# Kernel tuning notes

Hardware: AMD Instinct MI355X
Metric: run time of the kernel (lower is better)

Reference implementation:

```python
import math
import jax, jax.numpy as jnp
import numpy as np

B, T, N, S, D, H = 16, 64, 64, 4, 128, 8  # batch, enc steps, agents, state dim, lstm dim, heads


def _lin(k, i, o):
    return (jax.random.normal(k, (i, o), jnp.float32) / np.sqrt(i)).astype(jnp.float32)


def setup_inputs() -> dict:
    key = jax.random.key(0)
    ks = jax.random.split(key, 24)
    inp = {
        "x": jax.random.normal(ks[0], (B, T + 1, N, S), jnp.float32),
        # state_enc: S -> D
        "W_se": _lin(ks[1], S, D), "b_se": jnp.zeros((D,), jnp.float32),
        # init_hidden: S -> D (lstm_num = 1)
        "W_init": _lin(ks[2], S, D), "b_init": jnp.zeros((D,), jnp.float32),
        # GRU (1 layer): input D, hidden D; gates packed [r|z|n]
        "W_ih": _lin(ks[3], D, 3 * D), "W_hh": _lin(ks[4], D, 3 * D),
        "b_ih": jnp.zeros((3 * D,), jnp.float32), "b_hh": jnp.zeros((3 * D,), jnp.float32),
        # key_ct/query_ct/value_ct: D -> D, no bias (final_bias=False)
        "W_kc": _lin(ks[5], D, D), "W_qc": _lin(ks[6], D, D), "W_vc": _lin(ks[7], D, D),
        # gat attention: 2D -> 1
        "W_att": _lin(ks[8], 2 * D, 1), "b_att": jnp.zeros((1,), jnp.float32),
        # value: D -> D
        "W_val": _lin(ks[9], D, D), "b_val": jnp.zeros((D,), jnp.float32),
        # dec: 2D -> D
        "W_dec": _lin(ks[10], 2 * D, D), "b_dec": jnp.zeros((D,), jnp.float32),
        # mu/sig heads: D -> S
        "W_mu": _lin(ks[11], D, S), "b_mu": jnp.zeros((S,), jnp.float32),
        "W_sig": _lin(ks[12], D, S), "b_sig": jnp.zeros((S,), jnp.float32),
    }
    return inp


def _gru(xs, h0, W_ih, W_hh, b_ih, b_hh):
    # xs: [T, BN, D]; h0: [BN, D]. PyTorch GRU gate math.
    def step(h, x_t):
        gi = x_t @ W_ih + b_ih
        gh = h @ W_hh + b_hh
        ir, iz, inn = jnp.split(gi, 3, axis=-1)
        hr, hz, hn = jnp.split(gh, 3, axis=-1)
        r = jax.nn.sigmoid(ir + hr)
        z = jax.nn.sigmoid(iz + hz)
        n = jnp.tanh(inn + r * hn)
        h_new = (1.0 - z) * n + z * h
        return h_new, h_new
    hT, ys = jax.lax.scan(step, h0, xs)
    return ys, hT


def reference(x, W_se, b_se, W_init, b_init, W_ih, W_hh, b_ih, b_hh,
              W_kc, W_qc, W_vc, W_att, b_att, W_val, b_val,
              W_dec, b_dec, W_mu, b_mu, W_sig, b_sig):
    Bn, T1, Nn, Sn = x.shape
    Tn = T1 - 1
    Dn = W_se.shape[1]
    hd = Dn // H
    BN = Bn * Nn

    # initialize: h0 from first frame
    h0 = x[:, 0].reshape(BN, Sn) @ W_init + b_init  # [BN, D]

    # encode: state_enc + GRU over time
    xe = x[:, :-1] @ W_se + b_se                     # [B, T, N, D]
    xs = jnp.transpose(xe, (1, 0, 2, 3)).reshape(Tn, BN, Dn)
    ys, hT = _gru(xs, h0, W_ih, W_hh, b_ih, b_hh)    # ys: [T, BN, D]
    out = ys.reshape(Tn, Bn, Nn, Dn)

    # extract: per-pair temporal attention (pa=True)
    k = (out @ W_kc).reshape(Tn, Bn, Nn, H, hd)
    q = (out @ W_qc).reshape(Tn, Bn, Nn, H, hd)
    v = (out @ W_vc).reshape(Tn, Bn, Nn, H, hd)
    # score[b,h,i,j,t] = q[t,b,j]·k[t,b,i] / sqrt(D); softmax over t
    score = jnp.einsum('tbjhd,tbihd->bhijt', q, k) / math.sqrt(Dn)
    a = jax.nn.softmax(score, axis=-1)
    ctx = jnp.einsum('bhijt,tbihd->bhijd', a, v)     # [B,H,N,N,hd]
    ctx = jnp.transpose(ctx, (0, 2, 3, 1, 4)).reshape(Bn, Nn, Nn, Dn)

    # gat edge weight with tanh activation and zeroed diagonal
    w = jnp.concatenate([ctx, jnp.swapaxes(ctx, 1, 2)], axis=-1)  # [B,N,N,2D]
    e = (w @ W_att + b_att)[..., 0]
    weight = jnp.tanh(e + 0.5) * (1.0 - jnp.eye(Nn, dtype=x.dtype))

    # decode one step with last frame
    xd = (x[:, -1].reshape(BN, Sn) @ W_se + b_se)[None]  # [1, BN, D]
    _, h2 = _gru(xd, hT, W_ih, W_hh, b_ih, b_hh)
    bvec = h2.reshape(Bn, Nn, Dn)
    vv = bvec @ W_val + b_val
    p = jnp.einsum('bij,bjd->bid', weight, vv) / Nn      # gat: divide by agent_num
    c = jnp.concatenate([vv, p], axis=-1)
    d = c @ W_dec + b_dec
    mu = d @ W_mu + b_mu
    sig = jax.nn.sigmoid(d @ W_sig + b_sig) + 1e-6       # reg_norm = 1.0
    return mu, sig
```

## Files before the change

### kernel.cpp

```cpp
#include <hip/hip_runtime.h>
#include <math.h>

#define Bb 16
#define Tt 64
#define Nn 64
#define Ss 4
#define Dd 128
#define Hh 8
#define HD 16
#define BN 1024
#define G3 384

#define OFF_WX   0
#define OFF_BX   1536
#define OFF_YS   4096
#define OFF_KH   (OFF_YS + Tt*BN*Dd)
#define OFF_QH   (OFF_KH + Bb*Hh*Tt*Nn*HD/2)
#define OFF_VW1  (OFF_QH + Bb*Hh*Tt*Nn*HD/2)
#define OFF_VW2  (OFF_VW1 + Bb*Hh*Tt*Nn)
#define OFF_E    (OFF_VW2 + Bb*Hh*Tt*Nn)
#define OFF_VV   (OFF_E + Bb*Nn*Nn)
#define OFF_WKQ  (OFF_VV + BN*Dd)
#define OFF_WT   (OFF_WKQ + 17408)
#define OFF_WDF  (OFF_WT + 24576)
#define OFF_WMF  (OFF_WDF + 16384)
#define WS_FLOATS (OFF_WMF + 1024)

typedef _Float16 half2_t __attribute__((ext_vector_type(2)));
typedef _Float16 f16x8 __attribute__((ext_vector_type(8)));
typedef float f32x4 __attribute__((ext_vector_type(4)));

__device__ __forceinline__ float fast_sigmoid(float v) {
  return 1.f / (1.f + __expf(-v));
}
__device__ __forceinline__ float fast_tanh(float v) {
  float e2 = __expf(2.f * v);
  return 1.f - 2.f / (e2 + 1.f);
}

__global__ __launch_bounds__(384) void k_precompute(
    const float* __restrict__ W_se, const float* __restrict__ b_se,
    const float* __restrict__ W_ih, const float* __restrict__ b_ih,
    const float* __restrict__ W_hh,
    const float* __restrict__ W_kc, const float* __restrict__ W_qc,
    const float* __restrict__ W_vc, const float* __restrict__ W_att,
    const float* __restrict__ W_dec, const float* __restrict__ W_mu,
    const float* __restrict__ W_sig,
    float* __restrict__ ws) {
  const int tid = threadIdx.x;
  if (blockIdx.x == 50) {
    _Float16* WF = (_Float16*)(ws + OFF_WMF);
    for (int idx = tid; idx < 4*64*8; idx += 384) {
      int ks = idx >> 9, l = (idx >> 3) & 63, j = idx & 7;
      int k = ks*32 + (l >> 4)*8 + j;
      int c16 = l & 15;
      float v = (c16 < 4) ? W_mu[(size_t)k*Ss + c16]
              : ((c16 < 8) ? W_sig[(size_t)k*Ss + c16 - 4] : 0.f);
      WF[(size_t)(ks*64 + l)*8 + j] = (_Float16)v;
    }
    return;
  }
  if (blockIdx.x >= 42) {
    const int nt = blockIdx.x - 42;
    _Float16* WF = (_Float16*)(ws + OFF_WDF);
    for (int idx = tid; idx < 8*64*8; idx += 384) {
      int ks = idx >> 9, l = (idx >> 3) & 63, j = idx & 7;
      int k = ks*32 + (l >> 4)*8 + j;
      int c = nt*16 + (l & 15);
      WF[(size_t)((nt*8 + ks)*64 + l)*8 + j] = (_Float16)W_dec[(size_t)k*Dd + c];
    }
    return;
  }
  if (blockIdx.x >= 25) {
    const int nt = blockIdx.x - 25;
    _Float16* WF = (_Float16*)(ws + OFF_WKQ);
    for (int idx = tid; idx < 4*64*8; idx += 384) {
      int ks = idx >> 9, l = (idx >> 3) & 63, j = idx & 7;
      int k = ks*32 + (l >> 4)*8 + j;
      int c16 = l & 15;
      float v;
      if (nt < 16) {
        int cg = nt*16 + c16;
        v = (cg < Dd) ? W_kc[(size_t)k*Dd + cg] : W_qc[(size_t)k*Dd + cg - Dd];
      } else {
        int h = c16 >> 1, which = c16 & 1;
        float s = 0.f;
        for (int d = 0; d < HD; ++d)
          s = fmaf(W_vc[(size_t)k*Dd + h*HD + d], W_att[which*Dd + h*HD + d], s);
        v = s;
      }
      WF[(size_t)((nt*4 + ks)*64 + l)*8 + j] = (_Float16)v;
    }
    return;
  }
  if (blockIdx.x > 0) {
    const int nt = blockIdx.x - 1;
    _Float16* WF = (_Float16*)(ws + OFF_WT);
    for (int idx = tid; idx < 4*64*8; idx += 384) {
      int ks = idx >> 9, l = (idx >> 3) & 63, j = idx & 7;
      int k = ks*32 + (l >> 4)*8 + j;
      int c = nt*16 + (l & 15);
      WF[(size_t)((nt*4 + ks)*64 + l)*8 + j] = (_Float16)W_hh[(size_t)k*G3 + c];
    }
    return;
  }
  const int c = tid;
  float* Wx = ws + OFF_WX; float* bx = ws + OFF_BX;
  float accb = b_ih[c];
  float a0 = 0.f, a1 = 0.f, a2 = 0.f, a3 = 0.f;
  for (int k = 0; k < Dd; ++k) {
    float w = W_ih[k*G3 + c];
    accb = fmaf(b_se[k], w, accb);
    a0 = fmaf(W_se[0*Dd + k], w, a0);
    a1 = fmaf(W_se[1*Dd + k], w, a1);
    a2 = fmaf(W_se[2*Dd + k], w, a2);
    a3 = fmaf(W_se[3*Dd + k], w, a3);
  }
  bx[c] = accb;
  Wx[0*G3 + c] = a0; Wx[1*G3 + c] = a1; Wx[2*G3 + c] = a2; Wx[3*G3 + c] = a3;
}

__global__ __launch_bounds__(512, 2) void k_gru(
    const float* __restrict__ x, const float* __restrict__ W_init,
    const float* __restrict__ b_init,
    const float* __restrict__ b_hh, float* __restrict__ ws) {
  __shared__ __align__(16) _Float16 h_l[4][Dd + 8];
  __shared__ float gg[4][G3];
  __shared__ float xt_l[Tt+1][4][Ss];
  const int tid = threadIdx.x;
  const int wave = tid >> 6;
  const int lane = tid & 63;
  const int l15 = lane & 15;
  const int lk = lane >> 4;
  const int blk = blockIdx.x;
  const int row0 = blk * 4;
  const int b = row0 >> 6;
  const int n0 = row0 & 63;
  float* ys = ws + OFF_YS;
  const float* Wx = ws + OFF_WX;
  const float* bxp = ws + OFF_BX;

  const f16x8* WF = (const f16x8*)(ws + OFF_WT);
  f16x8 wf[3][4];
  #pragma unroll
  for (int i = 0; i < 3; ++i)
    #pragma unroll
    for (int ks = 0; ks < 4; ++ks)
      wf[i][ks] = WF[(size_t)((wave*3 + i)*4 + ks)*64 + lane];
  float br[3];
  #pragma unroll
  for (int i = 0; i < 3; ++i) br[i] = b_hh[(wave*3 + i)*16 + l15];

  const int row = tid >> 7, d = tid & 127;
  float wxr[3][4], bx3[3];
  #pragma unroll
  for (int g = 0; g < 3; ++g) {
    bx3[g] = bxp[g*Dd + d];
    #pragma unroll
    for (int s = 0; s < 4; ++s) wxr[g][s] = Wx[s*G3 + g*Dd + d];
  }

  for (int idx = tid; idx < (Tt+1)*4*Ss; idx += 512) {
    int t = idx >> 4, r = (idx >> 2) & 3, s = idx & 3;
    xt_l[t][r][s] = x[((size_t)(b*(Tt+1) + t)*Nn + (n0 + r))*Ss + s];
  }
  __syncthreads();

  float hprev;
  {
    float h0 = b_init[d];
    #pragma unroll
    for (int s = 0; s < Ss; ++s)
      h0 = fmaf(xt_l[0][row][s], W_init[s*Dd + d], h0);
    hprev = h0;
    h_l[row][d] = (_Float16)h0;
  }
  __syncthreads();

  for (int t = 0; t < Tt; ++t) {
    f16x8 af[4];
    #pragma unroll
    for (int ks = 0; ks < 4; ++ks)
      af[ks] = *(const f16x8*)&h_l[l15 & 3][ks*32 + lk*8];
    #pragma unroll
    for (int i = 0; i < 3; ++i) {
      f32x4 acc = {br[i], br[i], br[i], br[i]};
      #pragma unroll
      for (int ks = 0; ks < 4; ++ks)
        acc = __builtin_amdgcn_mfma_f32_16x16x32_f16(af[ks], wf[i][ks], acc, 0, 0, 0);
      if (lane < 16) {
        const int col = (wave*3 + i)*16 + l15;
        gg[0][col] = acc[0];
        gg[1][col] = acc[1];
        gg[2][col] = acc[2];
        gg[3][col] = acc[3];
      }
    }
    __syncthreads();
    {
      float gi_r = bx3[0], gi_z = bx3[1], gi_n = bx3[2];
      #pragma unroll
      for (int s = 0; s < 4; ++s) {
        float xv = xt_l[t][row][s];
        gi_r = fmaf(xv, wxr[0][s], gi_r);
        gi_z = fmaf(xv, wxr[1][s], gi_z);
        gi_n = fmaf(xv, wxr[2][s], gi_n);
      }
      float rg = fast_sigmoid(gi_r + gg[row][d]);
      float zg = fast_sigmoid(gi_z + gg[row][Dd + d]);
      float ng = fast_tanh(fmaf(rg, gg[row][2*Dd + d], gi_n));
      float hnew = fmaf(zg, hprev - ng, ng);
      hprev = hnew;
      h_l[row][d] = (_Float16)hnew;
      ys[(size_t)(t*BN + row0 + row)*Dd + d] = hnew;
    }
    __syncthreads();
  }
}

__global__ __launch_bounds__(256, 2) void k_kqv(float* __restrict__ ws) {
  __shared__ __align__(16) _Float16 ysl[64][136];
  const int tid = threadIdx.x;
  const int blk = blockIdx.x;
  const int b = blk >> 6, t = blk & 63;
  const int wave = tid >> 6, lane = tid & 63;
  const int l15 = lane & 15, lk = lane >> 4;

  const f16x8* WKQ = (const f16x8*)(ws + OFF_WKQ);
  f16x8 bf0[4], bf1[4], bf2[4], bf3[4], bu[4];
  #pragma unroll
  for (int ks = 0; ks < 4; ++ks) {
    bf0[ks] = WKQ[(size_t)((wave*4 + 0)*4 + ks)*64 + lane];
    bf1[ks] = WKQ[(size_t)((wave*4 + 1)*4 + ks)*64 + lane];
    bf2[ks] = WKQ[(size_t)((wave*4 + 2)*4 + ks)*64 + lane];
    bf3[ks] = WKQ[(size_t)((wave*4 + 3)*4 + ks)*64 + lane];
    bu[ks]  = WKQ[(size_t)(16*4 + ks)*64 + lane];
  }

  const float* ysrc = ws + OFF_YS + ((size_t)t*BN + b*64)*Dd;
  for (int idx = tid; idx < 64*16; idx += 256) {
    int r = idx >> 4, k8 = (idx & 15) * 8;
    float4 v0 = *(const float4*)&ysrc[r*Dd + k8];
    float4 v1 = *(const float4*)&ysrc[r*Dd + k8 + 4];
    f16x8 hv;
    hv[0] = (_Float16)v0.x; hv[1] = (_Float16)v0.y;
    hv[2] = (_Float16)v0.z; hv[3] = (_Float16)v0.w;
    hv[4] = (_Float16)v1.x; hv[5] = (_Float16)v1.y;
    hv[6] = (_Float16)v1.z; hv[7] = (_Float16)v1.w;
    *(f16x8*)&ysl[r][k8] = hv;
  }
  __syncthreads();

  _Float16* khd = (_Float16*)(ws + OFF_KH);
  _Float16* qhd = (_Float16*)(ws + OFF_QH);

  #pragma unroll
  for (int mt = 0; mt < 4; ++mt) {
    f16x8 af[4];
    #pragma unroll
    for (int ks = 0; ks < 4; ++ks)
      af[ks] = *(const f16x8*)&ysl[mt*16 + l15][ks*32 + lk*8];
    f32x4 a0 = {0.f,0.f,0.f,0.f}, a1 = a0, a2 = a0, a3 = a0;
    #pragma unroll
    for (int ks = 0; ks < 4; ++ks) {
      a0 = __builtin_amdgcn_mfma_f32_16x16x32_f16(af[ks], bf0[ks], a0, 0, 0, 0);
      a1 = __builtin_amdgcn_mfma_f32_16x16x32_f16(af[ks], bf1[ks], a1, 0, 0, 0);
      a2 = __builtin_amdgcn_mfma_f32_16x16x32_f16(af[ks], bf2[ks], a2, 0, 0, 0);
      a3 = __builtin_amdgcn_mfma_f32_16x16x32_f16(af[ks], bf3[ks], a3, 0, 0, 0);
    }
    const int rowb = mt*16 + lk*4;
    #pragma unroll
    for (int nti = 0; nti < 4; ++nti) {
      f32x4 av = (nti == 0) ? a0 : (nti == 1) ? a1 : (nti == 2) ? a2 : a3;
      const int gc = wave*64 + nti*16 + l15;
      const int hh = (gc >> 4) & 7;
      const int dd2 = gc & 15;
      _Float16* base = (gc < Dd) ? khd : qhd;
      const size_t rowbase = ((size_t)(b*Hh + hh)*Tt + t)*Nn*HD;
      #pragma unroll
      for (int rg2 = 0; rg2 < 4; ++rg2)
        base[rowbase + (size_t)(rowb + rg2)*HD + dd2] = (_Float16)av[rg2];
    }
    if (wave == 3) {
      f32x4 au = {0.f,0.f,0.f,0.f};
      #pragma unroll
      for (int ks = 0; ks < 4; ++ks)
        au = __builtin_amdgcn_mfma_f32_16x16x32_f16(af[ks], bu[ks], au, 0, 0, 0);
      const int h = l15 >> 1, which = l15 & 1;
      float* vw = ws + (which ? OFF_VW2 : OFF_VW1) + ((size_t)(b*Hh + h)*Tt + t)*Nn;
      #pragma unroll
      for (int rg2 = 0; rg2 < 4; ++rg2)
        vw[rowb + rg2] = au[rg2];
    }
  }
}

__global__ __launch_bounds__(1024) void k_attn(float* __restrict__ ws) {
  __shared__ float vw1_l[Tt][Nn];
  __shared__ float vw2_l[Tt][Nn];
  const int tid = threadIdx.x;
  const int bh = blockIdx.x;
  const int b = bh >> 3;
  const int wave = tid >> 6;
  const int it = wave >> 2, jt = wave & 3;
  const int i0 = it*16, j0 = jt*16;
  const int lane = tid & 63;
  const int l15 = lane & 15, lk = lane >> 4;
  const _Float16* kh = (const _Float16*)(ws + OFF_KH) + (size_t)bh*Tt*Nn*HD;
  const _Float16* qh = (const _Float16*)(ws + OFF_QH) + (size_t)bh*Tt*Nn*HD;
  const float* vw1 = ws + OFF_VW1 + (size_t)bh*Tt*Nn;
  const float* vw2 = ws + OFF_VW2 + (size_t)bh*Tt*Nn;
  float* e = ws + OFF_E + (size_t)b*Nn*Nn;
  const float scale = 0.08838834764831845f;

  #pragma unroll
  for (int s = 0; s < 4; ++s) {
    int idx = tid + s*1024;
    ((float*)vw1_l)[idx] = vw1[idx];
    ((float*)vw2_l)[idx] = vw2[idx];
  }
  __syncthreads();

  float S[4] = {0.f,0.f,0.f,0.f};
  float A1[4] = {0.f,0.f,0.f,0.f};
  float A2[4] = {0.f,0.f,0.f,0.f};
  const bool realk = (lk < 2);

  #pragma unroll 4
  for (int t = 0; t < Tt; ++t) {
    f16x8 af = {0,0,0,0,0,0,0,0}, bf = {0,0,0,0,0,0,0,0};
    if (realk) {
      af = *(const f16x8*)&kh[((size_t)t*Nn + i0 + l15)*HD + lk*8];
      bf = *(const f16x8*)&qh[((size_t)t*Nn + j0 + l15)*HD + lk*8];
    }
    f32x4 sc = {0.f,0.f,0.f,0.f};
    sc = __builtin_amdgcn_mfma_f32_16x16x32_f16(af, bf, sc, 0, 0, 0);
    float4 w1 = *(const float4*)&vw1_l[t][i0 + lk*4];
    float4 w2 = *(const float4*)&vw2_l[t][i0 + lk*4];
    const float* w1p = (const float*)&w1;
    const float* w2p = (const float*)&w2;
    #pragma unroll
    for (int r = 0; r < 4; ++r) {
      float s = fminf(fmaxf(sc[r] * scale, -60.f), 60.f);
      float ee = __expf(s);
      S[r] += ee;
      A1[r] = fmaf(ee, w1p[r], A1[r]);
      A2[r] = fmaf(ee, w2p[r], A2[r]);
    }
  }
  {
    const int j = j0 + l15;
    #pragma unroll
    for (int r = 0; r < 4; ++r) {
      const int i = i0 + lk*4 + r;
      float inv = 1.f / S[r];
      atomicAdd(&e[i*Nn + j], A1[r] * inv);
      atomicAdd(&e[j*Nn + i], A2[r] * inv);
    }
  }
}

__global__ __launch_bounds__(384) void k_decode(
    const float* __restrict__ x, const float* __restrict__ W_hh,
    const float* __restrict__ b_hh, const float* __restrict__ W_val,
    const float* __restrict__ b_val, float* __restrict__ ws) {
  __shared__ float h_lds[4][Dd];
  __shared__ float g_lds[4][4*Dd];
  __shared__ float xt[4][Ss];
  const int tid = threadIdx.x;
  const int blk = blockIdx.x;
  const int row0 = blk * 4;
  const int b = row0 >> 6;
  const int n0 = row0 & 63;
  const float* ys = ws + OFF_YS;
  const float* Wx = ws + OFF_WX;
  const float* bxp = ws + OFF_BX;
  if (tid < Dd) {
    for (int r = 0; r < 4; ++r)
      h_lds[r][tid] = ys[(size_t)((Tt-1)*BN + row0 + r)*Dd + tid];
  }
  if (tid >= 320 && tid < 336) {
    int q = tid - 320; int r = q >> 2, s = q & 3;
    xt[r][s] = x[((size_t)(b*(Tt+1) + Tt)*Nn + (n0 + r))*Ss + s];
  }
  const int c = tid;
  const float bhh = b_hh[c];
  const float wx0 = Wx[0*G3 + c], wx1 = Wx[1*G3 + c], wx2 = Wx[2*G3 + c], wx3 = Wx[3*G3 + c];
  const float bxv = bxp[c];
  __syncthreads();
  float acc[4] = {bhh, bhh, bhh, bhh};
  for (int k = 0; k < Dd; k += 4) {
    float w0 = W_hh[(k+0)*G3 + c];
    float w1 = W_hh[(k+1)*G3 + c];
    float w2 = W_hh[(k+2)*G3 + c];
    float w3 = W_hh[(k+3)*G3 + c];
    #pragma unroll
    for (int r = 0; r < 4; ++r) {
      float4 hv = *(const float4*)&h_lds[r][k];
      acc[r] = fmaf(hv.x, w0, acc[r]);
      acc[r] = fmaf(hv.y, w1, acc[r]);
      acc[r] = fmaf(hv.z, w2, acc[r]);
      acc[r] = fmaf(hv.w, w3, acc[r]);
    }
  }
  float gi[4];
  #pragma unroll
  for (int r = 0; r < 4; ++r) {
    float g = bxv;
    g = fmaf(xt[r][0], wx0, g);
    g = fmaf(xt[r][1], wx1, g);
    g = fmaf(xt[r][2], wx2, g);
    g = fmaf(xt[r][3], wx3, g);
    gi[r] = g;
  }
  if (c < 2*Dd) {
    #pragma unroll
    for (int r = 0; r < 4; ++r) g_lds[r][c] = acc[r] + gi[r];
  } else {
    #pragma unroll
    for (int r = 0; r < 4; ++r) { g_lds[r][c] = gi[r]; g_lds[r][c + Dd] = acc[r]; }
  }
  __syncthreads();
  if (tid < Dd) {
    const int d = tid;
    #pragma unroll
    for (int r = 0; r < 4; ++r) {
      float rg = fast_sigmoid(g_lds[r][d]);
      float zg = fast_sigmoid(g_lds[r][Dd + d]);
      float ng = fast_tanh(fmaf(rg, g_lds[r][3*Dd + d], g_lds[r][2*Dd + d]));
      float hn = fmaf(zg, h_lds[r][d] - ng, ng);
      h_lds[r][d] = hn;
    }
  }
  __syncthreads();
  if (tid < Dd) {
    const int c2 = tid;
    for (int r = 0; r < 4; ++r) {
      float a = b_val[c2];
      for (int k = 0; k < Dd; k += 4) {
        float4 hv = *(const float4*)&h_lds[r][k];
        a = fmaf(hv.x, W_val[(k+0)*Dd + c2], a);
        a = fmaf(hv.y, W_val[(k+1)*Dd + c2], a);
        a = fmaf(hv.z, W_val[(k+2)*Dd + c2], a);
        a = fmaf(hv.w, W_val[(k+3)*Dd + c2], a);
      }
      ws[OFF_VV + (size_t)(row0 + r)*Dd + c2] = a;
    }
  }
}

__global__ __launch_bounds__(256) void k_final(
    const float* __restrict__ b_dec, const float* __restrict__ b_mu,
    const float* __restrict__ b_sig, const float* __restrict__ b_att,
    float* __restrict__ ws, float* __restrict__ out) {
  __shared__ __align__(16) _Float16 vvT[Dd][72];
  __shared__ __align__(16) _Float16 wl[16][72];
  __shared__ __align__(16) _Float16 A2[16][264];
  __shared__ __align__(16) _Float16 A3[16][136];
  const int tid = threadIdx.x;
  const int wave = tid >> 6, lane = tid & 63;
  const int l15 = lane & 15, lk = lane >> 4;
  const int blk = blockIdx.x;
  const int b = blk >> 2, iq = blk & 3, i0 = iq*16;
  const float* vv = ws + OFF_VV + (size_t)b*64*Dd;
  const float* e  = ws + OFF_E + (size_t)b*Nn*Nn;
  const float batt = b_att[0];

  for (int idx = tid; idx < 64*Dd/4; idx += 256) {
    int r = idx >> 5, k4 = (idx & 31)*4;
    float4 v = *(const float4*)&vv[r*Dd + k4];
    vvT[k4+0][r] = (_Float16)v.x;
    vvT[k4+1][r] = (_Float16)v.y;
    vvT[k4+2][r] = (_Float16)v.z;
    vvT[k4+3][r] = (_Float16)v.w;
    int rl = r - i0;
    if (rl >= 0 && rl < 16) {
      A2[rl][k4+0] = (_Float16)v.x;
      A2[rl][k4+1] = (_Float16)v.y;
      A2[rl][k4+2] = (_Float16)v.z;
      A2[rl][k4+3] = (_Float16)v.w;
    }
  }
  for (int idx = tid; idx < 16*64; idx += 256) {
    int il = idx >> 6, jj = idx & 63;
    int i = i0 + il;
    float v = (i == jj) ? 0.f : fast_tanh(e[i*Nn + jj] + batt + 0.5f);
    wl[il][jj] = (_Float16)v;
  }
  __syncthreads();

  {
    f16x8 a0 = *(const f16x8*)&wl[l15][lk*8];
    f16x8 a1 = *(const f16x8*)&wl[l15][32 + lk*8];
    #pragma unroll
    for (int q = 0; q < 2; ++q) {
      const int nt = wave*2 + q;
      f16x8 b0 = *(const f16x8*)&vvT[nt*16 + l15][lk*8];
      f16x8 b1 = *(const f16x8*)&vvT[nt*16 + l15][32 + lk*8];
      f32x4 acc = {0.f,0.f,0.f,0.f};
      acc = __builtin_amdgcn_mfma_f32_16x16x32_f16(a0, b0, acc, 0, 0, 0);
      acc = __builtin_amdgcn_mfma_f32_16x16x32_f16(a1, b1, acc, 0, 0, 0);
      #pragma unroll
      for (int r = 0; r < 4; ++r)
        A2[lk*4 + r][128 + nt*16 + l15] = (_Float16)(acc[r] * (1.f/64.f));
    }
  }
  __syncthreads();

  const f16x8* WDF = (const f16x8*)(ws + OFF_WDF);
  {
    f16x8 ad[8];
    #pragma unroll
    for (int ks = 0; ks < 8; ++ks)
      ad[ks] = *(const f16x8*)&A2[l15][ks*32 + lk*8];
    #pragma unroll
    for (int q = 0; q < 2; ++q) {
      const int nt = wave*2 + q;
      const float bias = b_dec[nt*16 + l15];
      f32x4 acc = {bias, bias, bias, bias};
      #pragma unroll
      for (int ks = 0; ks < 8; ++ks)
        acc = __builtin_amdgcn_mfma_f32_16x16x32_f16(
            ad[ks], WDF[(size_t)((nt*8 + ks)*64) + lane], acc, 0, 0, 0);
      #pragma unroll
      for (int r = 0; r < 4; ++r)
        A3[lk*4 + r][nt*16 + l15] = (_Float16)acc[r];
    }
  }
  __syncthreads();

  if (wave == 0) {
    const f16x8* WMF = (const f16x8*)(ws + OFF_WMF);
    f16x8 ah[4];
    #pragma unroll
    for (int ks = 0; ks < 4; ++ks)
      ah[ks] = *(const f16x8*)&A3[l15][ks*32 + lk*8];
    const float bias = (l15 < 4) ? b_mu[l15] : ((l15 < 8) ? b_sig[l15 - 4] : 0.f);
    f32x4 acc = {bias, bias, bias, bias};
    #pragma unroll
    for (int ks = 0; ks < 4; ++ks)
      acc = __builtin_amdgcn_mfma_f32_16x16x32_f16(
          ah[ks], WMF[(size_t)(ks*64) + lane], acc, 0, 0, 0);
    if (l15 < 8) {
      const int which = l15 >> 2, s = l15 & 3;
      #pragma unroll
      for (int r = 0; r < 4; ++r) {
        float v = acc[r];
        if (which) v = 1.f/(1.f + __expf(-v)) + 1e-6f;
        out[(size_t)which*(Bb*Nn*Ss) + (size_t)(b*64 + i0 + lk*4 + r)*Ss + s] = v;
      }
    }
  }
}

extern "C" void kernel_launch(void* const* d_in, const int* in_sizes, int n_in,
                              void* d_out, int out_size, void* d_ws, size_t ws_size,
                              hipStream_t stream) {
  const float* x     = (const float*)d_in[0];
  const float* W_se  = (const float*)d_in[1];
  const float* b_se  = (const float*)d_in[2];
  const float* W_init= (const float*)d_in[3];
  const float* b_init= (const float*)d_in[4];
  const float* W_ih  = (const float*)d_in[5];
  const float* W_hh  = (const float*)d_in[6];
  const float* b_ih  = (const float*)d_in[7];
  const float* b_hh  = (const float*)d_in[8];
  const float* W_kc  = (const float*)d_in[9];
  const float* W_qc  = (const float*)d_in[10];
  const float* W_vc  = (const float*)d_in[11];
  const float* W_att = (const float*)d_in[12];
  const float* b_att = (const float*)d_in[13];
  const float* W_val = (const float*)d_in[14];
  const float* b_val = (const float*)d_in[15];
  const float* W_dec = (const float*)d_in[16];
  const float* b_dec = (const float*)d_in[17];
  const float* W_mu  = (const float*)d_in[18];
  const float* b_mu  = (const float*)d_in[19];
  const float* W_sig = (const float*)d_in[20];
  const float* b_sig = (const float*)d_in[21];
  float* ws = (float*)d_ws;
  float* out = (float*)d_out;

  if (ws_size < (size_t)WS_FLOATS * sizeof(float)) return;

  hipMemsetAsync(ws + OFF_E, 0, (size_t)Bb*Nn*Nn*sizeof(float), stream);
  k_precompute<<<51, 384, 0, stream>>>(W_se, b_se, W_ih, b_ih, W_hh, W_kc, W_qc,
                                       W_vc, W_att, W_dec, W_mu, W_sig, ws);
  k_gru<<<BN/4, 512, 0, stream>>>(x, W_init, b_init, b_hh, ws);
  k_kqv<<<Bb*Tt, 256, 0, stream>>>(ws);
  k_attn<<<Bb*Hh, 1024, 0, stream>>>(ws);
  k_decode<<<BN/4, 384, 0, stream>>>(x, W_hh, b_hh, W_val, b_val, ws);
  k_final<<<Bb*4, 256, 0, stream>>>(b_dec, b_mu, b_sig, b_att, ws, out);
}
```

Baseline: 139.1 us.

## Restructure GRU to 2 rows per block with in-register gate math and fp16 ys

The GRU recurrence kernel now handles 2 rows per 256-thread block instead of 4 rows per 512 threads, giving 512 blocks. Each wave computes two column tiles for all three gates, and the gate nonlinearities are applied straight from MFMA accumulators. This removes the gg LDS round trip and one __syncthreads per step, and double-buffers the hidden state. The ys history is now stored as fp16, which halves its write and read traffic, and k_kqv and k_decode read it directly without conversion. In exchange, only a quarter of the lanes do the elementwise work, the MFMA rows are mostly padding, and ys carries less precision.

Result: slower. 175.1 us (+25.9%).

```diff
diff --git a/kernel.cpp b/kernel.cpp
--- a/kernel.cpp
+++ b/kernel.cpp
@@ -120,99 +120,113 @@
   Wx[0*G3 + c] = a0; Wx[1*G3 + c] = a1; Wx[2*G3 + c] = a2; Wx[3*G3 + c] = a3;
 }
 
-__global__ __launch_bounds__(512, 2) void k_gru(
+__global__ __launch_bounds__(256, 2) void k_gru(
     const float* __restrict__ x, const float* __restrict__ W_init,
     const float* __restrict__ b_init,
     const float* __restrict__ b_hh, float* __restrict__ ws) {
-  __shared__ __align__(16) _Float16 h_l[4][Dd + 8];
-  __shared__ float gg[4][G3];
-  __shared__ float xt_l[Tt+1][4][Ss];
+  __shared__ __align__(16) _Float16 h_l[2][2][160];
+  __shared__ float xt_l[Tt+1][2][Ss];
   const int tid = threadIdx.x;
   const int wave = tid >> 6;
   const int lane = tid & 63;
-  const int l15 = lane & 15;
-  const int lk = lane >> 4;
+  const int l15 = lane & 15, lk = lane >> 4;
   const int blk = blockIdx.x;
-  const int row0 = blk * 4;
-  const int b = row0 >> 6;
-  const int n0 = row0 & 63;
-  float* ys = ws + OFF_YS;
+  const int row0 = blk * 2;
+  const int b = row0 >> 6, n0 = row0 & 63;
+  _Float16* ys = (_Float16*)(ws + OFF_YS);
   const float* Wx = ws + OFF_WX;
   const float* bxp = ws + OFF_BX;
 
   const f16x8* WF = (const f16x8*)(ws + OFF_WT);
-  f16x8 wf[3][4];
+  f16x8 wf[3][2][4];
+  float br[3][2], bx3[3][2], wxr[3][2][4];
   #pragma unroll
-  for (int i = 0; i < 3; ++i)
+  for (int g = 0; g < 3; ++g)
+    #pragma unroll
+    for (int u = 0; u < 2; ++u) {
+      const int nt = g*8 + wave*2 + u;
+      #pragma unroll
+      for (int ks = 0; ks < 4; ++ks)
+        wf[g][u][ks] = WF[(size_t)((nt*4 + ks)*64) + lane];
+      const int c = g*Dd + (wave*2 + u)*16 + l15;
+      br[g][u] = b_hh[c];
+      bx3[g][u] = bxp[c];
+      #pragma unroll
+      for (int s = 0; s < 4; ++s) wxr[g][u][s] = Wx[s*G3 + c];
+    }
+
+  for (int idx = tid; idx < (Tt+1)*2*Ss; idx += 256) {
+    int t = idx >> 3, r = (idx >> 2) & 1, s = idx & 3;
+    xt_l[t][r][s] = x[((size_t)(b*(Tt+1) + t)*Nn + (n0 + r))*Ss + s];
+  }
+  __syncthreads();
+
+  float hprev[2][2] = {{0.f,0.f},{0.f,0.f}};
+  if (lk == 0) {
+    #pragma unroll
+    for (int u = 0; u < 2; ++u) {
+      const int d = wave*32 + u*16 + l15;
+      #pragma unroll
+      for (int r = 0; r < 2; ++r) {
+        float h0 = b_init[d];
+        #pragma unroll
+        for (int s = 0; s < Ss; ++s)
+          h0 = fmaf(xt_l[0][r][s], W_init[s*Dd + d], h0);
+        hprev[u][r] = h0;
+        h_l[0][r][d] = (_Float16)h0;
+      }
+    }
+  }
+  __syncthreads();
+
+  for (int t = 0; t < Tt; ++t) {
+    const int cur = t & 1, nxt = cur ^ 1;
+    f16x8 af[4];
     #pragma unroll
     for (int ks = 0; ks < 4; ++ks)
-      wf[i][ks] = WF[(size_t)((wave*3 + i)*4 + ks)*64 + lane];
-  float br[3];
-  #pragma unroll
-  for (int i = 0; i < 3; ++i) br[i] = b_hh[(wave*3 + i)*16 + l15];
-
-  const int row = tid >> 7, d = tid & 127;
-  float wxr[3][4], bx3[3];
-  #pragma unroll
-  for (int g = 0; g < 3; ++g) {
-    bx3[g] = bxp[g*Dd + d];
-    #pragma unroll
-    for (int s = 0; s < 4; ++s) wxr[g][s] = Wx[s*G3 + g*Dd + d];
-  }
-
-  for (int idx = tid; idx < (Tt+1)*4*Ss; idx += 512) {
-    int t = idx >> 4, r = (idx >> 2) & 3, s = idx & 3;
-    xt_l[t][r][s] = x[((size_t)(b*(Tt+1) + t)*Nn + (n0 + r))*Ss + s];
-  }
-  __syncthreads();
-
-  float hprev;
-  {
-    float h0 = b_init[d];
-    #pragma unroll
-    for (int s = 0; s < Ss; ++s)
-      h0 = fmaf(xt_l[0][row][s], W_init[s*Dd + d], h0);
-    hprev = h0;
-    h_l[row][d] = (_Float16)h0;
-  }
-  __syncthreads();
-
-  for (int t = 0; t < Tt; ++t) {
-    f16x8 af[4];
-    #pragma unroll
-    for (int ks = 0; ks < 4; ++ks)
-      af[ks] = *(const f16x8*)&h_l[l15 & 3][ks*32 + lk*8];
-    #pragma unroll
-    for (int i = 0; i < 3; ++i) {
-      f32x4 acc = {br[i], br[i], br[i], br[i]};
-      #pragma unroll
-      for (int ks = 0; ks < 4; ++ks)
-        acc = __builtin_amdgcn_mfma_f32_16x16x32_f16(af[ks], wf[i][ks], acc, 0, 0, 0);
-      if (lane < 16) {
-        const int col = (wave*3 + i)*16 + l15;
-        gg[0][col] = acc[0];
-        gg[1][col] = acc[1];
-        gg[2][col] = acc[2];
-        gg[3][col] = acc[3];
+      af[ks] = *(const f16x8*)&h_l[cur][l15 & 1][ks*32 + lk*8];
+    f32x4 a00 = {br[0][0],br[0][0],br[0][0],br[0][0]};
+    f32x4 a01 = {br[0][1],br[0][1],br[0][1],br[0][1]};
+    f32x4 a10 = {br[1][0],br[1][0],br[1][0],br[1][0]};
+    f32x4 a11 = {br[1][1],br[1][1],br[1][1],br[1][1]};
+    f32x4 a20 = {br[2][0],br[2][0],br[2][0],br[2][0]};
+    f32x4 a21 = {br[2][1],br[2][1],br[2][1],br[2][1]};
+    #pragma unroll
+    for (int ks = 0; ks < 4; ++ks) {
+      a00 = __builtin_amdgcn_mfma_f32_16x16x32_f16(af[ks], wf[0][0][ks], a00, 0, 0, 0);
+      a01 = __builtin_amdgcn_mfma_f32_16x16x32_f16(af[ks], wf[0][1][ks], a01, 0, 0, 0);
+      a10 = __builtin_amdgcn_mfma_f32_16x16x32_f16(af[ks], wf[1][0][ks], a10, 0, 0, 0);
+      a11 = __builtin_amdgcn_mfma_f32_16x16x32_f16(af[ks], wf[1][1][ks], a11, 0, 0, 0);
+      a20 = __builtin_amdgcn_mfma_f32_16x16x32_f16(af[ks], wf[2][0][ks], a20, 0, 0, 0);
+      a21 = __builtin_amdgcn_mfma_f32_16x16x32_f16(af[ks], wf[2][1][ks], a21, 0, 0, 0);
+    }
+    if (lk == 0) {
+      #pragma unroll
+      for (int u = 0; u < 2; ++u) {
+        const int d = wave*32 + u*16 + l15;
+        const f32x4& ar = u ? a01 : a00;
+        const f32x4& az = u ? a11 : a10;
+        const f32x4& an = u ? a21 : a20;
+        #pragma unroll
+        for (int r = 0; r < 2; ++r) {
+          float x0 = xt_l[t][r][0], x1 = xt_l[t][r][1];
+          float x2 = xt_l[t][r][2], x3 = xt_l[t][r][3];
+          float gi_r = bx3[0][u], gi_z = bx3[1][u], gi_n = bx3[2][u];
+          gi_r = fmaf(x0, wxr[0][u][0], gi_r); gi_r = fmaf(x1, wxr[0][u][1], gi_r);
+          gi_r = fmaf(x2, wxr[0][u][2], gi_r); gi_r = fmaf(x3, wxr[0][u][3], gi_r);
+          gi_z = fmaf(x0, wxr[1][u][0], gi_z); gi_z = fmaf(x1, wxr[1][u][1], gi_z);
+          gi_z = fmaf(x2, wxr[1][u][2], gi_z); gi_z = fmaf(x3, wxr[1][u][3], gi_z);
+          gi_n = fmaf(x0, wxr[2][u][0], gi_n); gi_n = fmaf(x1, wxr[2][u][1], gi_n);
+          gi_n = fmaf(x2, wxr[2][u][2], gi_n); gi_n = fmaf(x3, wxr[2][u][3], gi_n);
+          float rg = fast_sigmoid(gi_r + ar[r]);
+          float zg = fast_sigmoid(gi_z + az[r]);
+          float ng = fast_tanh(fmaf(rg, an[r], gi_n));
+          float hn = fmaf(zg, hprev[u][r] - ng, ng);
+          hprev[u][r] = hn;
+          h_l[nxt][r][d] = (_Float16)hn;
+          ys[(size_t)(t*BN + row0 + r)*Dd + d] = (_Float16)hn;
+        }
       }
-    }
-    __syncthreads();
-    {
-      float gi_r = bx3[0], gi_z = bx3[1], gi_n = bx3[2];
-      #pragma unroll
-      for (int s = 0; s < 4; ++s) {
-        float xv = xt_l[t][row][s];
-        gi_r = fmaf(xv, wxr[0][s], gi_r);
-        gi_z = fmaf(xv, wxr[1][s], gi_z);
-        gi_n = fmaf(xv, wxr[2][s], gi_n);
-      }
-      float rg = fast_sigmoid(gi_r + gg[row][d]);
-      float zg = fast_sigmoid(gi_z + gg[row][Dd + d]);
-      float ng = fast_tanh(fmaf(rg, gg[row][2*Dd + d], gi_n));
-      float hnew = fmaf(zg, hprev - ng, ng);
-      hprev = hnew;
-      h_l[row][d] = (_Float16)hnew;
-      ys[(size_t)(t*BN + row0 + row)*Dd + d] = hnew;
     }
     __syncthreads();
   }
@@ -237,17 +251,11 @@
     bu[ks]  = WKQ[(size_t)(16*4 + ks)*64 + lane];
   }
 
-  const float* ysrc = ws + OFF_YS + ((size_t)t*BN + b*64)*Dd;
-  for (int idx = tid; idx < 64*16; idx += 256) {
-    int r = idx >> 4, k8 = (idx & 15) * 8;
-    float4 v0 = *(const float4*)&ysrc[r*Dd + k8];
-    float4 v1 = *(const float4*)&ysrc[r*Dd + k8 + 4];
-    f16x8 hv;
-    hv[0] = (_Float16)v0.x; hv[1] = (_Float16)v0.y;
-    hv[2] = (_Float16)v0.z; hv[3] = (_Float16)v0.w;
-    hv[4] = (_Float16)v1.x; hv[5] = (_Float16)v1.y;
-    hv[6] = (_Float16)v1.z; hv[7] = (_Float16)v1.w;
-    *(f16x8*)&ysl[r][k8] = hv;
+  const _Float16* ysrc = (const _Float16*)(ws + OFF_YS) + ((size_t)t*BN + b*64)*Dd;
+  for (int idx = tid; idx < 64*8; idx += 256) {
+    int r = idx >> 3, k16 = (idx & 7)*16;
+    *(f16x8*)&ysl[r][k16]     = *(const f16x8*)&ysrc[r*Dd + k16];
+    *(f16x8*)&ysl[r][k16 + 8] = *(const f16x8*)&ysrc[r*Dd + k16 + 8];
   }
   __syncthreads();
 
@@ -372,12 +380,12 @@
   const int row0 = blk * 4;
   const int b = row0 >> 6;
   const int n0 = row0 & 63;
-  const float* ys = ws + OFF_YS;
+  const _Float16* ysf = (const _Float16*)(ws + OFF_YS);
   const float* Wx = ws + OFF_WX;
   const float* bxp = ws + OFF_BX;
   if (tid < Dd) {
     for (int r = 0; r < 4; ++r)
-      h_lds[r][tid] = ys[(size_t)((Tt-1)*BN + row0 + r)*Dd + tid];
+      h_lds[r][tid] = (float)ysf[(size_t)((Tt-1)*BN + row0 + r)*Dd + tid];
   }
   if (tid >= 320 && tid < 336) {
     int q = tid - 320; int r = q >> 2, s = q & 3;
@@ -586,7 +594,7 @@
   hipMemsetAsync(ws + OFF_E, 0, (size_t)Bb*Nn*Nn*sizeof(float), stream);
   k_precompute<<<51, 384, 0, stream>>>(W_se, b_se, W_ih, b_ih, W_hh, W_kc, W_qc,
                                        W_vc, W_att, W_dec, W_mu, W_sig, ws);
-  k_gru<<<BN/4, 512, 0, stream>>>(x, W_init, b_init, b_hh, ws);
+  k_gru<<<BN/2, 256, 0, stream>>>(x, W_init, b_init, b_hh, ws);
   k_kqv<<<Bb*Tt, 256, 0, stream>>>(ws);
   k_attn<<<Bb*Hh, 1024, 0, stream>>>(ws);
   k_decode<<<BN/4, 384, 0, stream>>>(x, W_hh, b_hh, W_val, b_val, ws);
```
